# Kernel tuning notes

Measured on AMD Instinct MI355X. Metric: run time of the kernel, lower is better.

The kernel has to match this reference:

```python
import jax, jax.numpy as jnp
import numpy as np

WINDOW_SIZE = 11
SIGMA = 1.5
C1 = 0.01 ** 2
C2 = 0.03 ** 2


def _gaussian_window(window_size, num_channels, dtype=jnp.float32):
    x = np.arange(window_size)
    k = np.exp(-((x - window_size // 2) ** 2) / (2.0 * SIGMA ** 2))
    k = k / k.sum()
    k2d = np.outer(k, k).astype(np.float32)
    # (C, 1, K, K) depthwise kernel, same Gaussian per channel
    w = np.broadcast_to(k2d, (num_channels, 1, window_size, window_size))
    return jnp.asarray(np.ascontiguousarray(w), dtype=dtype)


def _depthwise_conv(x, window):
    # x: (N,C,H,W), window: (C,1,K,K); groups=C, SAME-ish padding = K//2
    pad = window.shape[-1] // 2
    return jax.lax.conv_general_dilated(
        x, window,
        window_strides=(1, 1),
        padding=[(pad, pad), (pad, pad)],
        dimension_numbers=("NCHW", "OIHW", "NCHW"),
        feature_group_count=x.shape[1],
    )


def setup_inputs() -> dict:
    key = jax.random.key(0)
    k1, k2 = jax.random.split(key)
    shape = (16, 3, 512, 512)
    img1 = jax.random.uniform(k1, shape, dtype=jnp.float32)
    img2 = jax.random.uniform(k2, shape, dtype=jnp.float32)
    window = _gaussian_window(WINDOW_SIZE, shape[1])
    return {"img1": img1, "img2": img2, "window": window}


def reference(img1, img2, window):
    mu1 = _depthwise_conv(img1, window)
    mu2 = _depthwise_conv(img2, window)
    mu1_sq = mu1 * mu1
    mu2_sq = mu2 * mu2
    mu1_mu2 = mu1 * mu2
    sigma1_sq = _depthwise_conv(img1 * img1, window) - mu1_sq
    sigma2_sq = _depthwise_conv(img2 * img2, window) - mu2_sq
    sigma12 = _depthwise_conv(img1 * img2, window) - mu1_mu2
    ssim_map = ((2.0 * mu1_mu2 + C1) * (2.0 * sigma12 + C2)) / (
        (mu1_sq + mu2_sq + C1) * (sigma1_sq + sigma2_sq + C2)
    )
    return jnp.mean(ssim_map)  # size_average=True
```

## Files before the change

kernel.cpp:

```cpp
#include <hip/hip_runtime.h>


#define KSZ   11
#define PAD   5
#define TILE  32
#define HALO  42
#define SXW   44
#define NT    256
#define NBX   16
#define NBY   16
#define NPLANES 48
#define NBLOCKS (NBX * NBY * NPLANES)

struct W11 { float w[KSZ]; };

static __device__ __forceinline__ float fast_rcp(float x) {
#if __has_builtin(__builtin_amdgcn_rcpf)
    return __builtin_amdgcn_rcpf(x);
#else
    return 1.0f / x;
#endif
}

__global__ __launch_bounds__(NT)
void ssim_fused(const float* __restrict__ img1,
                const float* __restrict__ img2,
                const float* __restrict__ window,
                double* __restrict__ acc)
{
    __shared__ float k1d[KSZ];
    __shared__ __align__(16) float2 sx[HALO * SXW];
    __shared__ __align__(16) float2 hA[HALO * TILE];
    __shared__ __align__(16) float2 hC[HALO * TILE];
    __shared__ __align__(16) float  hD[HALO * TILE];
    __shared__ float red[NT / 64];

    const int tid = threadIdx.x;
    const int bx = blockIdx.x * TILE;
    const int by = blockIdx.y * TILE;
    const size_t planeOff = (size_t)blockIdx.z * 512 * 512;
    const float* p1 = img1 + planeOff;
    const float* p2 = img2 + planeOff;

    if (tid < KSZ) {
        float s = 0.f;
        #pragma unroll
        for (int j = 0; j < KSZ; ++j) s += window[tid * KSZ + j];
        k1d[tid] = s;
    }

    for (int idx = tid; idx < HALO * HALO; idx += NT) {
        const int r = idx / HALO;
        const int c = idx - r * HALO;
        const int gr = by + r - PAD;
        const int gc = bx + c - PAD;
        float v1 = 0.f, v2 = 0.f;
        if (((unsigned)gr < 512u) && ((unsigned)gc < 512u)) {
            const size_t g = (size_t)gr * 512 + gc;
            v1 = p1[g];
            v2 = p2[g];
        }
        sx[r * SXW + c] = make_float2(v1, v2);
    }
    __syncthreads();

    W11 wk;
    #pragma unroll
    for (int k = 0; k < KSZ; ++k) wk.w[k] = k1d[k];

    for (int s = tid; s < HALO * 16; s += NT) {
        const int r  = s >> 4;
        const int g  = s & 15;
        const int c0 = g * 2;
        const float2* row = sx + r * SXW + c0;
        const float2 x0 = row[0],  x1 = row[1],  x2 = row[2],  x3 = row[3];
        const float2 x4 = row[4],  x5 = row[5],  x6 = row[6],  x7 = row[7];
        const float2 x8 = row[8],  x9 = row[9],  x10 = row[10], x11 = row[11];

        float2 m0 = make_float2(0.f, 0.f), m1 = make_float2(0.f, 0.f);
        float2 e0 = make_float2(0.f, 0.f), e1 = make_float2(0.f, 0.f);
        float  d0 = 0.f, d1 = 0.f;

#define HTAP(K, A, B)                                                   \
        {                                                               \
            const float w = wk.w[K];                                    \
            m0.x += w * (A).x;       m0.y += w * (A).y;                 \
            e0.x += w * (A).x*(A).x; e0.y += w * (A).y*(A).y;           \
            d0   += w * (A).x*(A).y;                                    \
            m1.x += w * (B).x;       m1.y += w * (B).y;                 \
            e1.x += w * (B).x*(B).x; e1.y += w * (B).y*(B).y;           \
            d1   += w * (B).x*(B).y;                                    \
        }
        HTAP(0,  x0,  x1)  HTAP(1,  x1,  x2)  HTAP(2,  x2,  x3)
        HTAP(3,  x3,  x4)  HTAP(4,  x4,  x5)  HTAP(5,  x5,  x6)
        HTAP(6,  x6,  x7)  HTAP(7,  x7,  x8)  HTAP(8,  x8,  x9)
        HTAP(9,  x9,  x10) HTAP(10, x10, x11)
#undef HTAP

        const int base = r * TILE + c0;
        *(float4*)(&hA[base]) = make_float4(m0.x, m0.y, m1.x, m1.y);
        *(float4*)(&hC[base]) = make_float4(e0.x, e0.y, e1.x, e1.y);
        *(float2*)(&hD[base]) = make_float2(d0, d1);
    }
    __syncthreads();

    const float C1f = 1e-4f;
    const float C2f = 9e-4f;
    float lsum = 0.f;
    {
        const int vc  = tid & 31;
        const int vr0 = (tid >> 5) * 4;

        float2 mu0 = make_float2(0.f,0.f), mu1 = make_float2(0.f,0.f),
               mu2 = make_float2(0.f,0.f), mu3 = make_float2(0.f,0.f);
        float2 ee0 = make_float2(0.f,0.f), ee1 = make_float2(0.f,0.f),
               ee2 = make_float2(0.f,0.f), ee3 = make_float2(0.f,0.f);
        float  dd0 = 0.f, dd1 = 0.f, dd2 = 0.f, dd3 = 0.f;

#define VTAP(J, I, MU, EE, DD)                                          \
        if ((J) >= (I) && (J) - (I) < KSZ) {                            \
            const float w = wk.w[((J) >= (I)) ? (J) - (I) : 0];         \
            MU.x += w * a.x; MU.y += w * a.y;                           \
            EE.x += w * c.x; EE.y += w * c.y;                           \
            DD   += w * d;                                              \
        }
#define VROW(J)                                                         \
        {                                                               \
            const int hr = vr0 + (J);                                   \
            const float2 a = hA[hr * TILE + vc];                        \
            const float2 c = hC[hr * TILE + vc];                        \
            const float  d = hD[hr * TILE + vc];                        \
            VTAP(J, 0, mu0, ee0, dd0)                                   \
            VTAP(J, 1, mu1, ee1, dd1)                                   \
            VTAP(J, 2, mu2, ee2, dd2)                                   \
            VTAP(J, 3, mu3, ee3, dd3)                                   \
        }
        VROW(0)  VROW(1)  VROW(2)  VROW(3)  VROW(4)  VROW(5)  VROW(6)
        VROW(7)  VROW(8)  VROW(9)  VROW(10) VROW(11) VROW(12) VROW(13)
#undef VROW
#undef VTAP

#define SSIMI(MU, EE, DD)                                               \
        {                                                               \
            const float mu1v = MU.x, mu2v = MU.y;                       \
            const float mu1sq = mu1v * mu1v;                            \
            const float mu2sq = mu2v * mu2v;                            \
            const float mu12  = mu1v * mu2v;                            \
            const float s11 = EE.x - mu1sq;                             \
            const float s22 = EE.y - mu2sq;                             \
            const float s12 = DD   - mu12;                              \
            const float num = (2.f * mu12 + C1f) * (2.f * s12 + C2f);   \
            const float den = (mu1sq + mu2sq + C1f) * (s11 + s22 + C2f);\
            lsum += num * fast_rcp(den);                                \
        }
        SSIMI(mu0, ee0, dd0)
        SSIMI(mu1, ee1, dd1)
        SSIMI(mu2, ee2, dd2)
        SSIMI(mu3, ee3, dd3)
#undef SSIMI
    }

    #pragma unroll
    for (int off = 32; off > 0; off >>= 1)
        lsum += __shfl_down(lsum, off, 64);
    const int wave = tid >> 6;
    const int lane = tid & 63;
    if (lane == 0) red[wave] = lsum;
    __syncthreads();
    if (tid == 0) {
        const float bsum = red[0] + red[1] + red[2] + red[3];
        atomicAdd(acc, (double)bsum);
    }
}

__global__ __launch_bounds__(64)
void ssim_finalize(const double* __restrict__ acc, float* __restrict__ out) {
    if (threadIdx.x == 0)
        out[0] = (float)(acc[0] * (1.0 / ((double)NBLOCKS * TILE * TILE)));
}

extern "C" void kernel_launch(void* const* d_in, const int* in_sizes, int n_in,
                              void* d_out, int out_size, void* d_ws, size_t ws_size,
                              hipStream_t stream) {
    const float* img1   = (const float*)d_in[0];
    const float* img2   = (const float*)d_in[1];
    const float* window = (const float*)d_in[2];
    float* out = (float*)d_out;
    double* acc = (double*)d_ws;

    hipMemsetAsync(d_ws, 0, 8, stream);

    dim3 grid(NBX, NBY, NPLANES);
    ssim_fused<<<grid, NT, 0, stream>>>(img1, img2, window, acc);
    ssim_finalize<<<1, 64, 0, stream>>>(acc, out);
}
```

Baseline: 264.4 us.

## Alias horizontal-pass buffers onto input tile and pack mean/energy as float4

Shared memory is merged into one buffer: the horizontal-pass outputs overwrite the input halo tile after a barrier, with each thread holding its up to three slot results in registers across that barrier. Mean and second-moment values are interleaved into one float4 per pixel, so the vertical pass issues one 16-byte LDS read instead of two 8-byte reads. The aim is a smaller LDS footprint per block, allowing more resident blocks, plus fewer LDS instructions. The cost is an extra barrier and more live registers in the horizontal stage.

```diff
diff --git a/kernel.cpp b/kernel.cpp
--- a/kernel.cpp
+++ b/kernel.cpp
@@ -11,8 +11,10 @@
 #define NBY   16
 #define NPLANES 48
 #define NBLOCKS (NBX * NBY * NPLANES)
+#define NSLOT  (HALO * 16)
 
 struct W11 { float w[KSZ]; };
+struct HRes { float2 m0, m1, e0, e1; float d0, d1; };
 
 static __device__ __forceinline__ float fast_rcp(float x) {
 #if __has_builtin(__builtin_amdgcn_rcpf)
@@ -22,18 +24,56 @@
 #endif
 }
 
+static __device__ __forceinline__ HRes hslot(const float2* sxp, const W11& wk, int s) {
+    const int r  = s >> 4;
+    const int g  = s & 15;
+    const float2* row = sxp + r * SXW + 2 * g;
+    const float2 x0 = row[0],  x1 = row[1],  x2 = row[2],  x3 = row[3];
+    const float2 x4 = row[4],  x5 = row[5],  x6 = row[6],  x7 = row[7];
+    const float2 x8 = row[8],  x9 = row[9],  x10 = row[10], x11 = row[11];
+    HRes o;
+    o.m0 = make_float2(0.f, 0.f); o.m1 = make_float2(0.f, 0.f);
+    o.e0 = make_float2(0.f, 0.f); o.e1 = make_float2(0.f, 0.f);
+    o.d0 = 0.f; o.d1 = 0.f;
+#define HTAP(K, A, B)                                                   \
+    {                                                                   \
+        const float w = wk.w[K];                                        \
+        o.m0.x += w * (A).x;       o.m0.y += w * (A).y;                 \
+        o.e0.x += w * (A).x*(A).x; o.e0.y += w * (A).y*(A).y;           \
+        o.d0   += w * (A).x*(A).y;                                      \
+        o.m1.x += w * (B).x;       o.m1.y += w * (B).y;                 \
+        o.e1.x += w * (B).x*(B).x; o.e1.y += w * (B).y*(B).y;           \
+        o.d1   += w * (B).x*(B).y;                                      \
+    }
+    HTAP(0,  x0,  x1)  HTAP(1,  x1,  x2)  HTAP(2,  x2,  x3)
+    HTAP(3,  x3,  x4)  HTAP(4,  x4,  x5)  HTAP(5,  x5,  x6)
+    HTAP(6,  x6,  x7)  HTAP(7,  x7,  x8)  HTAP(8,  x8,  x9)
+    HTAP(9,  x9,  x10) HTAP(10, x10, x11)
+#undef HTAP
+    return o;
+}
+
+static __device__ __forceinline__ void hwrite(float4* hA, float* hD, const HRes& o, int s) {
+    const int r = s >> 4;
+    const int g = s & 15;
+    const int base = r * TILE + 2 * g;
+    hA[base]     = make_float4(o.m0.x, o.m0.y, o.e0.x, o.e0.y);
+    hA[base + 1] = make_float4(o.m1.x, o.m1.y, o.e1.x, o.e1.y);
+    *(float2*)(hD + base) = make_float2(o.d0, o.d1);
+}
+
 __global__ __launch_bounds__(NT)
 void ssim_fused(const float* __restrict__ img1,
                 const float* __restrict__ img2,
                 const float* __restrict__ window,
                 double* __restrict__ acc)
 {
+    __shared__ __align__(16) float smem[HALO * TILE * 5];
     __shared__ float k1d[KSZ];
-    __shared__ __align__(16) float2 sx[HALO * SXW];
-    __shared__ __align__(16) float2 hA[HALO * TILE];
-    __shared__ __align__(16) float2 hC[HALO * TILE];
-    __shared__ __align__(16) float  hD[HALO * TILE];
     __shared__ float red[NT / 64];
+    float2* sx = (float2*)smem;
+    float4* hA = (float4*)smem;
+    float*  hD = smem + HALO * TILE * 4;
 
     const int tid = threadIdx.x;
     const int bx = blockIdx.x * TILE;
@@ -68,40 +108,16 @@
     #pragma unroll
     for (int k = 0; k < KSZ; ++k) wk.w[k] = k1d[k];
 
-    for (int s = tid; s < HALO * 16; s += NT) {
-        const int r  = s >> 4;
-        const int g  = s & 15;
-        const int c0 = g * 2;
-        const float2* row = sx + r * SXW + c0;
-        const float2 x0 = row[0],  x1 = row[1],  x2 = row[2],  x3 = row[3];
-        const float2 x4 = row[4],  x5 = row[5],  x6 = row[6],  x7 = row[7];
-        const float2 x8 = row[8],  x9 = row[9],  x10 = row[10], x11 = row[11];
-
-        float2 m0 = make_float2(0.f, 0.f), m1 = make_float2(0.f, 0.f);
-        float2 e0 = make_float2(0.f, 0.f), e1 = make_float2(0.f, 0.f);
-        float  d0 = 0.f, d1 = 0.f;
-
-#define HTAP(K, A, B)                                                   \
-        {                                                               \
-            const float w = wk.w[K];                                    \
-            m0.x += w * (A).x;       m0.y += w * (A).y;                 \
-            e0.x += w * (A).x*(A).x; e0.y += w * (A).y*(A).y;           \
-            d0   += w * (A).x*(A).y;                                    \
-            m1.x += w * (B).x;       m1.y += w * (B).y;                 \
-            e1.x += w * (B).x*(B).x; e1.y += w * (B).y*(B).y;           \
-            d1   += w * (B).x*(B).y;                                    \
-        }
-        HTAP(0,  x0,  x1)  HTAP(1,  x1,  x2)  HTAP(2,  x2,  x3)
-        HTAP(3,  x3,  x4)  HTAP(4,  x4,  x5)  HTAP(5,  x5,  x6)
-        HTAP(6,  x6,  x7)  HTAP(7,  x7,  x8)  HTAP(8,  x8,  x9)
-        HTAP(9,  x9,  x10) HTAP(10, x10, x11)
-#undef HTAP
-
-        const int base = r * TILE + c0;
-        *(float4*)(&hA[base]) = make_float4(m0.x, m0.y, m1.x, m1.y);
-        *(float4*)(&hC[base]) = make_float4(e0.x, e0.y, e1.x, e1.y);
-        *(float2*)(&hD[base]) = make_float2(d0, d1);
-    }
+    const bool has2 = (tid + 512) < NSLOT;
+    const HRes rA = hslot(sx, wk, tid);
+    const HRes rB = hslot(sx, wk, tid + 256);
+    HRes rC;
+    if (has2) rC = hslot(sx, wk, tid + 512);
+    __syncthreads();
+
+    hwrite(hA, hD, rA, tid);
+    hwrite(hA, hD, rB, tid + 256);
+    if (has2) hwrite(hA, hD, rC, tid + 512);
     __syncthreads();
 
     const float C1f = 1e-4f;
@@ -121,15 +137,14 @@
         if ((J) >= (I) && (J) - (I) < KSZ) {                            \
             const float w = wk.w[((J) >= (I)) ? (J) - (I) : 0];         \
             MU.x += w * a.x; MU.y += w * a.y;                           \
-            EE.x += w * c.x; EE.y += w * c.y;                           \
-            DD   += w * d;                                              \
+            EE.x += w * a.z; EE.y += w * a.w;                           \
+            DD   += w * dv;                                             \
         }
 #define VROW(J)                                                         \
         {                                                               \
             const int hr = vr0 + (J);                                   \
-            const float2 a = hA[hr * TILE + vc];                        \
-            const float2 c = hC[hr * TILE + vc];                        \
-            const float  d = hD[hr * TILE + vc];                        \
+            const float4 a  = hA[hr * TILE + vc];                       \
+            const float  dv = hD[hr * TILE + vc];                       \
             VTAP(J, 0, mu0, ee0, dd0)                                   \
             VTAP(J, 1, mu1, ee1, dd1)                                   \
             VTAP(J, 2, mu2, ee2, dd2)                                   \
```

After: 267.6 us. Within noise of the previous version (+1.2%).
